# Kernel optimization log

Measured on AMD Instinct MI355X. Metric: run time of the kernel, lower is better.

Reference implementation:

```python
import jax, jax.numpy as jnp
import numpy as np

# Cayley-Dickson octonion multiplication tables (from the source module)
SIGN_TABLE = np.array([
    [+1, -1, -1, -1, -1, -1, -1, -1],
    [+1, +1, +1, -1, +1, -1, -1, +1],
    [+1, -1, +1, +1, +1, +1, -1, -1],
    [+1, +1, -1, +1, +1, -1, +1, -1],
    [+1, -1, -1, -1, +1, +1, +1, +1],
    [+1, +1, -1, +1, -1, +1, -1, +1],
    [+1, +1, +1, -1, -1, +1, +1, -1],
    [+1, -1, +1, +1, -1, -1, +1, +1],
], dtype=np.float32)
WEIGHT_IDX = np.array([
    [0, 1, 2, 3, 4, 5, 6, 7],
    [1, 0, 3, 2, 5, 4, 7, 6],
    [2, 3, 0, 1, 6, 7, 4, 5],
    [3, 2, 1, 0, 7, 6, 5, 4],
    [4, 5, 6, 7, 0, 1, 2, 3],
    [5, 4, 7, 6, 1, 0, 3, 2],
    [6, 7, 4, 5, 2, 3, 0, 1],
    [7, 6, 5, 4, 3, 2, 1, 0],
], dtype=np.int32)

B, T, D_IN, D_OUT = 4, 2048, 4096, 4096
K = D_IN // 8   # per-component input dim
N = D_OUT // 8  # per-component output dim


def setup_inputs() -> dict:
    key = jax.random.key(0)
    k1, k2 = jax.random.split(key)
    x = jax.random.normal(k1, (B, T, D_IN), dtype=jnp.float32)
    weight = jax.random.normal(k2, (8, N, K), dtype=jnp.float32) * (1.0 / np.sqrt(K))
    return {"x": x, "weight": weight}


def reference(x, weight):
    """Fused octonion (Cayley-Dickson) linear layer.

    y_i = sum_j sign[i,j] * x_j @ W[widx[i,j]].T
    x components are contiguous chunks of the last dim: x_j = x[..., j*K:(j+1)*K].
    """
    b, t, f = x.shape
    k = f // 8
    xs = x.reshape(b, t, 8, k)                 # [B,T,8,K], component axis j
    Wg = weight[jnp.asarray(WEIGHT_IDX)]        # [8(i),8(j),N,K] gathered weights
    S = jnp.asarray(SIGN_TABLE, dtype=x.dtype)  # [8(i),8(j)]
    # contract over j (component) and k (features); produce [B,T,i,N]
    y = jnp.einsum('ij,btjk,ijnk->btin', S, xs, Wg)
    return y.reshape(b, t, -1)                  # [B,T,8*N]
```

## Files before the change

### kernel.cpp

```cpp
#include <hip/hip_runtime.h>
#include <stdint.h>

typedef __attribute__((ext_vector_type(8))) short bf16x8;
typedef __attribute__((ext_vector_type(4))) float f32x4;

#define D_IN  4096
#define D_OUT 4096
#define KC 512
#define NC 512
#define BM 128
#define BN 128
#define BK 64
#define NSTEP (D_IN / BK)

__constant__ float c_sign[64] = {
 +1,-1,-1,-1,-1,-1,-1,-1,
 +1,+1,+1,-1,+1,-1,-1,+1,
 +1,-1,+1,+1,+1,+1,-1,-1,
 +1,+1,-1,+1,+1,-1,+1,-1,
 +1,-1,-1,-1,+1,+1,+1,+1,
 +1,+1,-1,+1,-1,+1,-1,+1,
 +1,+1,+1,-1,-1,+1,+1,-1,
 +1,-1,+1,+1,-1,-1,+1,+1,
};

__device__ inline unsigned int pack2bf16(float a, float b) {
    unsigned int ua = __builtin_bit_cast(unsigned int, a);
    unsigned int ub = __builtin_bit_cast(unsigned int, b);
    ua = (ua + 0x7FFFu + ((ua >> 16) & 1u)) >> 16;
    ub = (ub + 0x7FFFu + ((ub >> 16) & 1u)) >> 16;
    return ua | (ub << 16);
}

typedef __attribute__((address_space(1))) const unsigned int gas_u32;
typedef __attribute__((address_space(3))) unsigned int las_u32;
#define ASYNC16(g, l) __builtin_amdgcn_global_load_lds((gas_u32*)(g), (las_u32*)(l), 16, 0, 0)


__global__ __launch_bounds__(256)
void conv_x(const float* __restrict__ in, unsigned short* __restrict__ out, int n8) {
    int i = blockIdx.x * blockDim.x + threadIdx.x;
    if (i >= n8) return;
    const float4 a = ((const float4*)in)[(size_t)i * 2];
    const float4 b = ((const float4*)in)[(size_t)i * 2 + 1];
    uint4 o;
    o.x = pack2bf16(a.x, a.y); o.y = pack2bf16(a.z, a.w);
    o.z = pack2bf16(b.x, b.y); o.w = pack2bf16(b.z, b.w);
    ((uint4*)out)[i] = o;
}

__global__ __launch_bounds__(256)
void conv_w(const float* __restrict__ W, unsigned short* __restrict__ out) {
    int gid = blockIdx.x * blockDim.x + threadIdx.x;
    int row = gid >> 9;
    int c8  = gid & 511;
    int i = row >> 9, n = row & 511;
    int j = c8 >> 6;
    int k = (c8 & 63) << 3;
    float sgn = c_sign[i * 8 + j];
    const float* src = W + ((((i ^ j) * NC + n) * KC) + k);
    float4 a = *(const float4*)(src);
    float4 b = *(const float4*)(src + 4);
    uint4 o;
    o.x = pack2bf16(a.x * sgn, a.y * sgn); o.y = pack2bf16(a.z * sgn, a.w * sgn);
    o.z = pack2bf16(b.x * sgn, b.y * sgn); o.w = pack2bf16(b.z * sgn, b.w * sgn);
    ((uint4*)out)[gid] = o;
}


__global__ __launch_bounds__(256)
void octo_gemm_bf16(const unsigned short* __restrict__ Xb,
                    const unsigned short* __restrict__ Wb,
                    float* __restrict__ Y, int M)
{
    __shared__ __align__(16) unsigned short As[BM * BK];
    __shared__ __align__(16) unsigned short Bs[BN * BK];

    const int tid  = threadIdx.x;
    const int lane = tid & 63;
    const int wave = tid >> 6;
    const int wr   = wave >> 1;
    const int wc   = wave & 1;

    const int nbn = D_OUT / BN;
    int bid = blockIdx.x;
    int cpx = (M / BM) * nbn >> 3;
    int wg  = (bid & 7) * cpx + (bid >> 3);
    const int bm = wg / nbn, bn = wg % nbn;
    const int row0 = bm * BM;
    const int col0 = bn * BN;

    const int sr = tid >> 3;
    const int sc = tid & 7;

    f32x4 acc[4][4];
    #pragma unroll
    for (int m = 0; m < 4; ++m)
        #pragma unroll
        for (int n = 0; n < 4; ++n)
            acc[m][n] = (f32x4){0.f, 0.f, 0.f, 0.f};

    const char* AsB = (const char*)As;
    const char* BsB = (const char*)Bs;

    for (int step = 0; step < NSTEP; ++step) {
        const int k0 = step * BK;
        if (step) __syncthreads();
        #pragma unroll
        for (int p = 0; p < 4; ++p) {
            const int r  = p * 32 + sr;
            const int cs = sc ^ (r & 7);
            ASYNC16(Xb + (size_t)(row0 + r) * D_IN + k0 + cs * 8,
                    As + p * 2048 + tid * 8);
            ASYNC16(Wb + (size_t)(col0 + r) * D_IN + k0 + cs * 8,
                    Bs + p * 2048 + tid * 8);
        }
        __syncthreads();

        #pragma unroll
        for (int kk = 0; kk < 2; ++kk) {
            bf16x8 af[4], bf[4];
            #pragma unroll
            for (int m = 0; m < 4; ++m) {
                const int r = wr * 64 + m * 16 + (lane & 15);
                const int chunk = (kk * 4 + (lane >> 4)) ^ (r & 7);
                af[m] = *(const bf16x8*)(AsB + r * 128 + (chunk << 4));
            }
            #pragma unroll
            for (int n = 0; n < 4; ++n) {
                const int r = wc * 64 + n * 16 + (lane & 15);
                const int chunk = (kk * 4 + (lane >> 4)) ^ (r & 7);
                bf[n] = *(const bf16x8*)(BsB + r * 128 + (chunk << 4));
            }
            #pragma unroll
            for (int m = 0; m < 4; ++m)
                #pragma unroll
                for (int n = 0; n < 4; ++n)
                    acc[m][n] = __builtin_amdgcn_mfma_f32_16x16x32_bf16(
                        af[m], bf[n], acc[m][n], 0, 0, 0);
        }
    }

    const int rl = (lane >> 4) << 2;
    const int cl = lane & 15;
    #pragma unroll
    for (int m = 0; m < 4; ++m) {
        const int rg = row0 + wr * 64 + m * 16 + rl;
        #pragma unroll
        for (int n = 0; n < 4; ++n) {
            const int cg = col0 + wc * 64 + n * 16 + cl;
            #pragma unroll
            for (int q = 0; q < 4; ++q)
                Y[(size_t)(rg + q) * D_OUT + cg] = acc[m][n][q];
        }
    }
}


__global__ __launch_bounds__(256)
void octo_gemm_f32(const float* __restrict__ X, const float* __restrict__ W,
                   float* __restrict__ Y, int M)
{
    __shared__ __align__(16) unsigned short As[BM * BK];
    __shared__ __align__(16) unsigned short Bs[BN * BK];

    const int tid  = threadIdx.x;
    const int lane = tid & 63;
    const int wave = tid >> 6;
    const int wr   = wave >> 1;
    const int wc   = wave & 1;

    const int nbn = D_OUT / BN;
    const int nwg = (M / BM) * nbn;
    int bid = blockIdx.x;
    int wg  = bid;
    if ((nwg & 7) == 0) {
        int cpx = nwg >> 3;
        wg = (bid & 7) * cpx + (bid >> 3);
    }
    const int bm = wg / nbn, bn = wg % nbn;
    const int row0  = bm * BM;
    const int col0  = bn * BN;
    const int icomp = col0 >> 9;
    const int noff  = col0 & (NC - 1);

    const int srow = tid >> 4;
    const int scol = (tid & 15) << 2;

    f32x4 acc[4][4];
    #pragma unroll
    for (int m = 0; m < 4; ++m)
        #pragma unroll
        for (int n = 0; n < 4; ++n)
            acc[m][n] = (f32x4){0.f, 0.f, 0.f, 0.f};

    char* AsB = (char*)As;
    char* BsB = (char*)Bs;
    const int byteC = scol << 1;

    for (int step = 0; step < NSTEP; ++step) {
        const int k0 = step * BK;
        const int j  = k0 >> 9;
        const int kc = k0 & (KC - 1);
        const float sgn = c_sign[icomp * 8 + j];
        const int   w   = icomp ^ j;
        const float* Wp = W + (((size_t)w * NC + noff) * KC + kc);
        const float* Xp = X + ((size_t)row0 * D_IN + k0);

        __syncthreads();
        #pragma unroll
        for (int p = 0; p < 8; ++p) {
            const int r  = p * 16 + srow;
            const int sb = r * 128 + ((((byteC >> 4) ^ (r & 7)) << 4)) + (byteC & 8);
            const float4 va = *(const float4*)(&Xp[(size_t)r * D_IN + scol]);
            *(uint2*)(AsB + sb) = make_uint2(pack2bf16(va.x, va.y),
                                             pack2bf16(va.z, va.w));
            const float4 vb = *(const float4*)(&Wp[(size_t)r * KC + scol]);
            *(uint2*)(BsB + sb) = make_uint2(pack2bf16(vb.x * sgn, vb.y * sgn),
                                             pack2bf16(vb.z * sgn, vb.w * sgn));
        }
        __syncthreads();

        #pragma unroll
        for (int kk = 0; kk < 2; ++kk) {
            bf16x8 af[4], bf[4];
            #pragma unroll
            for (int m = 0; m < 4; ++m) {
                const int r = wr * 64 + m * 16 + (lane & 15);
                const int chunk = (kk * 4 + (lane >> 4)) ^ (r & 7);
                af[m] = *(const bf16x8*)(AsB + r * 128 + (chunk << 4));
            }
            #pragma unroll
            for (int n = 0; n < 4; ++n) {
                const int r = wc * 64 + n * 16 + (lane & 15);
                const int chunk = (kk * 4 + (lane >> 4)) ^ (r & 7);
                bf[n] = *(const bf16x8*)(BsB + r * 128 + (chunk << 4));
            }
            #pragma unroll
            for (int m = 0; m < 4; ++m)
                #pragma unroll
                for (int n = 0; n < 4; ++n)
                    acc[m][n] = __builtin_amdgcn_mfma_f32_16x16x32_bf16(
                        af[m], bf[n], acc[m][n], 0, 0, 0);
        }
    }

    const int rl = (lane >> 4) << 2;
    const int cl = lane & 15;
    #pragma unroll
    for (int m = 0; m < 4; ++m) {
        const int rg = row0 + wr * 64 + m * 16 + rl;
        #pragma unroll
        for (int n = 0; n < 4; ++n) {
            const int cg = col0 + wc * 64 + n * 16 + cl;
            #pragma unroll
            for (int q = 0; q < 4; ++q)
                Y[(size_t)(rg + q) * D_OUT + cg] = acc[m][n][q];
        }
    }
}

extern "C" void kernel_launch(void* const* d_in, const int* in_sizes, int n_in,
                              void* d_out, int out_size, void* d_ws, size_t ws_size,
                              hipStream_t stream) {
    const float* X = (const float*)d_in[0];
    const float* W = (const float*)d_in[1];
    float* Y = (float*)d_out;
    const int M = in_sizes[0] / D_IN;
    const int nwg = (M / BM) * (D_OUT / BN);

    const size_t xb_bytes = (size_t)M * D_IN * sizeof(unsigned short);
    const size_t wb_bytes = (size_t)D_OUT * D_IN * sizeof(unsigned short);

    if (ws_size >= xb_bytes + wb_bytes) {
        unsigned short* Xb = (unsigned short*)d_ws;
        unsigned short* Wb = (unsigned short*)((char*)d_ws + xb_bytes);
        const int n8x = M * D_IN / 8;
        hipLaunchKernelGGL(conv_x, dim3(n8x / 256), dim3(256), 0, stream, X, Xb, n8x);
        hipLaunchKernelGGL(conv_w, dim3((D_OUT * D_IN / 8) / 256), dim3(256), 0, stream, W, Wb);
        hipLaunchKernelGGL(octo_gemm_bf16, dim3(nwg), dim3(256), 0, stream, Xb, Wb, Y, M);
    } else {
        hipLaunchKernelGGL(octo_gemm_f32, dim3(nwg), dim3(256), 0, stream, X, W, Y, M);
    }
}
```

Before: 314.7 us.

## Replace bf16 GEMM with 256x256 tile, 8-wave, 8-phase double-buffered pipeline

Replaces the single-buffered 128x128 bf16 MFMA GEMM with a 256x256 output tile computed by 512 threads (8 waves). K-tiles are double-buffered in LDS and loaded asynchronously in eight phases that overlap with MFMA work, using raw s_barrier, waitcnt and setprio scheduling. The goal is more reuse per loaded tile and hiding global-to-LDS latency behind compute. In exchange it uses 128 KB of LDS and more registers per thread, which lowers occupancy and makes the synchronisation hard to get right. The wrapped tile addressing also prefetches one redundant tile at the end.

```diff
diff --git a/kernel.cpp b/kernel.cpp
--- a/kernel.cpp
+++ b/kernel.cpp
@@ -8,10 +8,7 @@
 #define D_OUT 4096
 #define KC 512
 #define NC 512
-#define BM 128
-#define BN 128
-#define BK 64
-#define NSTEP (D_IN / BK)
+#define NT 64
 
 __constant__ float c_sign[64] = {
  +1,-1,-1,-1,-1,-1,-1,-1,
@@ -68,84 +65,140 @@
 }
 
 
-__global__ __launch_bounds__(256)
-void octo_gemm_bf16(const unsigned short* __restrict__ Xb,
-                    const unsigned short* __restrict__ Wb,
-                    float* __restrict__ Y, int M)
+template<int P>
+__device__ __forceinline__ void do_phase(
+    const unsigned short* bufA, const unsigned short* bufB,
+    f32x4 (&acc)[8][4], bf16x8 (&bfr)[4][2],
+    const unsigned short* stg_g, unsigned short* stg_l,
+    size_t goff0, size_t goff1, int loff0, int loff1,
+    int lane, int wr, int wc)
 {
-    __shared__ __align__(16) unsigned short As[BM * BK];
-    __shared__ __align__(16) unsigned short Bs[BN * BK];
+    bf16x8 afr[2][2];
+    #pragma unroll
+    for (int q = 0; q < 2; ++q) {
+        const int r = wr * 128 + (2 * P + q) * 16 + (lane & 15);
+        #pragma unroll
+        for (int kk = 0; kk < 2; ++kk) {
+            const int ch = (kk * 4 + (lane >> 4)) ^ (r & 7);
+            afr[q][kk] = *(const bf16x8*)((const char*)bufA + r * 128 + ch * 16);
+        }
+    }
+    if (P == 0) {
+        #pragma unroll
+        for (int n = 0; n < 4; ++n) {
+            const int r = wc * 64 + n * 16 + (lane & 15);
+            #pragma unroll
+            for (int kk = 0; kk < 2; ++kk) {
+                const int ch = (kk * 4 + (lane >> 4)) ^ (r & 7);
+                bfr[n][kk] = *(const bf16x8*)((const char*)bufB + r * 128 + ch * 16);
+            }
+        }
+    }
+    ASYNC16(stg_g + goff0, stg_l + loff0);
+    ASYNC16(stg_g + goff1, stg_l + loff1);
+    __builtin_amdgcn_s_barrier();
+    asm volatile("s_waitcnt lgkmcnt(0)");
+    __builtin_amdgcn_s_setprio(1);
+    #pragma unroll
+    for (int kk = 0; kk < 2; ++kk)
+        #pragma unroll
+        for (int q = 0; q < 2; ++q)
+            #pragma unroll
+            for (int n = 0; n < 4; ++n)
+                acc[2 * P + q][n] = __builtin_amdgcn_mfma_f32_16x16x32_bf16(
+                    afr[q][kk], bfr[n][kk], acc[2 * P + q][n], 0, 0, 0);
+    __builtin_amdgcn_s_setprio(0);
+}
+
+#define ENDP do { __builtin_amdgcn_s_barrier(); asm volatile("" ::: "memory"); } while (0)
+
+__global__ __launch_bounds__(512, 2)
+void octo_gemm_8ph(const unsigned short* __restrict__ Xb,
+                   const unsigned short* __restrict__ Wb,
+                   float* __restrict__ Y, int M)
+{
+    __shared__ __align__(16) unsigned short sm[65536];
+    unsigned short* A0 = sm;
+    unsigned short* A1 = sm + 16384;
+    unsigned short* B0 = sm + 32768;
+    unsigned short* B1 = sm + 49152;
 
     const int tid  = threadIdx.x;
     const int lane = tid & 63;
     const int wave = tid >> 6;
-    const int wr   = wave >> 1;
-    const int wc   = wave & 1;
-
-    const int nbn = D_OUT / BN;
+    const int wr   = wave >> 2;
+    const int wc   = wave & 3;
+
+    const int nbn = D_OUT / 256;
+    const int nwg = (M / 256) * nbn;
     int bid = blockIdx.x;
-    int cpx = (M / BM) * nbn >> 3;
+    int cpx = nwg >> 3;
     int wg  = (bid & 7) * cpx + (bid >> 3);
     const int bm = wg / nbn, bn = wg % nbn;
-    const int row0 = bm * BM;
-    const int col0 = bn * BN;
-
-    const int sr = tid >> 3;
-    const int sc = tid & 7;
-
-    f32x4 acc[4][4];
-    #pragma unroll
-    for (int m = 0; m < 4; ++m)
+    const int row0 = bm * 256, col0 = bn * 256;
+
+    const int srow  = tid >> 3;
+    const int sch   = tid & 7;
+    const size_t goff0 = (size_t)srow * D_IN + (size_t)((sch ^ (srow & 7)) * 8);
+    const size_t goff1 = goff0 + (size_t)64 * D_IN;
+    const int loff0 = tid * 8;
+    const int loff1 = loff0 + 4096;
+
+    const unsigned short* gX = Xb + (size_t)row0 * D_IN;
+    const unsigned short* gW = Wb + (size_t)col0 * D_IN;
+
+    f32x4 acc[8][4];
+    #pragma unroll
+    for (int m = 0; m < 8; ++m)
         #pragma unroll
         for (int n = 0; n < 4; ++n)
             acc[m][n] = (f32x4){0.f, 0.f, 0.f, 0.f};
 
-    const char* AsB = (const char*)As;
-    const char* BsB = (const char*)Bs;
-
-    for (int step = 0; step < NSTEP; ++step) {
-        const int k0 = step * BK;
-        if (step) __syncthreads();
-        #pragma unroll
-        for (int p = 0; p < 4; ++p) {
-            const int r  = p * 32 + sr;
-            const int cs = sc ^ (r & 7);
-            ASYNC16(Xb + (size_t)(row0 + r) * D_IN + k0 + cs * 8,
-                    As + p * 2048 + tid * 8);
-            ASYNC16(Wb + (size_t)(col0 + r) * D_IN + k0 + cs * 8,
-                    Bs + p * 2048 + tid * 8);
-        }
-        __syncthreads();
-
-        #pragma unroll
-        for (int kk = 0; kk < 2; ++kk) {
-            bf16x8 af[4], bf[4];
-            #pragma unroll
-            for (int m = 0; m < 4; ++m) {
-                const int r = wr * 64 + m * 16 + (lane & 15);
-                const int chunk = (kk * 4 + (lane >> 4)) ^ (r & 7);
-                af[m] = *(const bf16x8*)(AsB + r * 128 + (chunk << 4));
-            }
-            #pragma unroll
-            for (int n = 0; n < 4; ++n) {
-                const int r = wc * 64 + n * 16 + (lane & 15);
-                const int chunk = (kk * 4 + (lane >> 4)) ^ (r & 7);
-                bf[n] = *(const bf16x8*)(BsB + r * 128 + (chunk << 4));
-            }
-            #pragma unroll
-            for (int m = 0; m < 4; ++m)
-                #pragma unroll
-                for (int n = 0; n < 4; ++n)
-                    acc[m][n] = __builtin_amdgcn_mfma_f32_16x16x32_bf16(
-                        af[m], bf[n], acc[m][n], 0, 0, 0);
-        }
+    ASYNC16(gX + goff0, A0 + loff0);              ASYNC16(gX + goff1, A0 + loff1);
+    ASYNC16(gX + 128 * D_IN + goff0, A0 + 8192 + loff0);
+    ASYNC16(gX + 128 * D_IN + goff1, A0 + 8192 + loff1);
+    ASYNC16(gW + goff0, B0 + loff0);              ASYNC16(gW + goff1, B0 + loff1);
+    ASYNC16(gW + 128 * D_IN + goff0, B0 + 8192 + loff0);
+    ASYNC16(gW + 128 * D_IN + goff1, B0 + 8192 + loff1);
+    ASYNC16(gW + 64 + goff0, B1 + loff0);         ASYNC16(gW + 64 + goff1, B1 + loff1);
+    ASYNC16(gW + 64 + 128 * D_IN + goff0, B1 + 8192 + loff0);
+    ASYNC16(gW + 64 + 128 * D_IN + goff1, B1 + 8192 + loff1);
+    asm volatile("s_waitcnt vmcnt(4)");
+    ENDP;
+
+    bf16x8 bfr[4][2];
+    for (int i = 0; i < NT / 2; ++i) {
+        const int u = 2 * i;
+        const unsigned short* gA1t = gX + ((u + 1) & (NT - 1)) * 64;
+        const unsigned short* gA2t = gX + ((u + 2) & (NT - 1)) * 64;
+        const unsigned short* gB2t = gW + ((u + 2) & (NT - 1)) * 64;
+        const unsigned short* gB3t = gW + ((u + 3) & (NT - 1)) * 64;
+
+        do_phase<0>(A0, B0, acc, bfr, gA1t,            A1,        goff0, goff1, loff0, loff1, lane, wr, wc);
+        ENDP;
+        do_phase<1>(A0, B0, acc, bfr, gA1t + 128*D_IN, A1 + 8192, goff0, goff1, loff0, loff1, lane, wr, wc);
+        ENDP;
+        do_phase<2>(A0, B0, acc, bfr, gB2t,            B0,        goff0, goff1, loff0, loff1, lane, wr, wc);
+        ENDP;
+        do_phase<3>(A0, B0, acc, bfr, gB2t + 128*D_IN, B0 + 8192, goff0, goff1, loff0, loff1, lane, wr, wc);
+        asm volatile("s_waitcnt vmcnt(4)");
+        ENDP;
+        do_phase<0>(A1, B1, acc, bfr, gA2t,            A0,        goff0, goff1, loff0, loff1, lane, wr, wc);
+        ENDP;
+        do_phase<1>(A1, B1, acc, bfr, gA2t + 128*D_IN, A0 + 8192, goff0, goff1, loff0, loff1, lane, wr, wc);
+        ENDP;
+        do_phase<2>(A1, B1, acc, bfr, gB3t,            B1,        goff0, goff1, loff0, loff1, lane, wr, wc);
+        ENDP;
+        do_phase<3>(A1, B1, acc, bfr, gB3t + 128*D_IN, B1 + 8192, goff0, goff1, loff0, loff1, lane, wr, wc);
+        asm volatile("s_waitcnt vmcnt(4)");
+        ENDP;
     }
 
     const int rl = (lane >> 4) << 2;
     const int cl = lane & 15;
     #pragma unroll
-    for (int m = 0; m < 4; ++m) {
-        const int rg = row0 + wr * 64 + m * 16 + rl;
+    for (int m = 0; m < 8; ++m) {
+        const int rg = row0 + wr * 128 + m * 16 + rl;
         #pragma unroll
         for (int n = 0; n < 4; ++n) {
             const int cg = col0 + wc * 64 + n * 16 + cl;
@@ -156,6 +209,10 @@
     }
 }
 
+
+#define BM 128
+#define BN 128
+#define BK 64
 
 __global__ __launch_bounds__(256)
 void octo_gemm_f32(const float* __restrict__ X, const float* __restrict__ W,
@@ -198,7 +255,7 @@
     char* BsB = (char*)Bs;
     const int byteC = scol << 1;
 
-    for (int step = 0; step < NSTEP; ++step) {
+    for (int step = 0; step < NT; ++step) {
         const int k0 = step * BK;
         const int j  = k0 >> 9;
         const int kc = k0 & (KC - 1);
@@ -267,19 +324,20 @@
     const float* W = (const float*)d_in[1];
     float* Y = (float*)d_out;
     const int M = in_sizes[0] / D_IN;
-    const int nwg = (M / BM) * (D_OUT / BN);
 
     const size_t xb_bytes = (size_t)M * D_IN * sizeof(unsigned short);
     const size_t wb_bytes = (size_t)D_OUT * D_IN * sizeof(unsigned short);
 
-    if (ws_size >= xb_bytes + wb_bytes) {
+    if (ws_size >= xb_bytes + wb_bytes && (M % 256) == 0) {
         unsigned short* Xb = (unsigned short*)d_ws;
         unsigned short* Wb = (unsigned short*)((char*)d_ws + xb_bytes);
         const int n8x = M * D_IN / 8;
         hipLaunchKernelGGL(conv_x, dim3(n8x / 256), dim3(256), 0, stream, X, Xb, n8x);
         hipLaunchKernelGGL(conv_w, dim3((D_OUT * D_IN / 8) / 256), dim3(256), 0, stream, W, Wb);
-        hipLaunchKernelGGL(octo_gemm_bf16, dim3(nwg), dim3(256), 0, stream, Xb, Wb, Y, M);
+        const int nwg = (M / 256) * (D_OUT / 256);
+        hipLaunchKernelGGL(octo_gemm_8ph, dim3(nwg), dim3(512), 0, stream, Xb, Wb, Y, M);
     } else {
+        const int nwg = (M / BM) * (D_OUT / BN);
         hipLaunchKernelGGL(octo_gemm_f32, dim3(nwg), dim3(256), 0, stream, X, W, Y, M);
     }
 }
```

Result: faster. 263.5 us (-16.3%).
